# Optimization experiments

Hardware: AMD Instinct MI355X
Metric: run time of the kernel (lower is better)

## Reference

```python
import jax, jax.numpy as jnp
import numpy as np

B, N, F_IN, H = 16, 1024, 64, 256
NEG = -9e15
ALPHA = 0.2  # LeakyReLU slope


def _leaky(x):
    return jnp.where(x >= 0, x, ALPHA * x)


def setup_inputs() -> dict:
    key = jax.random.key(0)
    ks = jax.random.split(key, 12)
    s = lambda k, shape, fan: jax.random.normal(k, shape, jnp.float32) / np.sqrt(fan)
    node_features = jax.random.normal(ks[0], (B, N, F_IN), jnp.float32)
    adj_matrix = jax.random.randint(ks[1], (B, N, N), 0, 2).astype(jnp.float32)
    return {
        "node_features": node_features,
        "adj_matrix": adj_matrix,
        "emb_W": s(ks[2], (F_IN, H), F_IN),
        "emb_b": jnp.zeros((H,), jnp.float32),
        "W0": s(ks[3], (H, H), H),
        "a1_0": s(ks[4], (H,), H),
        "a2_0": s(ks[5], (H,), H),
        "W1": s(ks[6], (H, H), H),
        "a1_1": s(ks[7], (H,), H),
        "a2_1": s(ks[8], (H,), H),
        "gp_W1": s(ks[9], (H, H), H),
        "gp_b1": jnp.zeros((H,), jnp.float32),
        "gp_W2": s(ks[10], (H, H), H),
        "gp_b2": jnp.zeros((H,), jnp.float32),
    }


def _gat_layer(x, mask, W, a1, a2):
    # x: [B,N,H]; mask: [B,N,N] bool. Equivalent to original concat trick:
    # a([h_i || h_j]) = h_i @ a1 + h_j @ a2 with a.weight split in halves.
    h = jnp.einsum('bnf,fo->bno', x, W)              # [B,N,H]
    s1 = jnp.einsum('bnh,h->bn', h, a1)              # [B,N]
    s2 = jnp.einsum('bnh,h->bn', h, a2)              # [B,N]
    e = _leaky(s1[:, :, None] + s2[:, None, :])      # [B,N,N]
    att = jax.nn.softmax(jnp.where(mask, e, NEG), axis=2)
    # dropout p=0.2 is identity in eval mode
    return jnp.einsum('bij,bjh->bih', att, h)        # [B,N,H]


def reference(node_features, adj_matrix, emb_W, emb_b,
              W0, a1_0, a2_0, W1, a1_1, a2_1,
              gp_W1, gp_b1, gp_W2, gp_b2):
    mask = adj_matrix > 0
    x = jnp.einsum('bnf,fh->bnh', node_features, emb_W) + emb_b
    x = jax.nn.relu(_gat_layer(x, mask, W0, a1_0, a2_0))
    x = jax.nn.relu(_gat_layer(x, mask, W1, a1_1, a2_1))
    g = jnp.mean(x, axis=1) + jnp.max(x, axis=1)     # [B,H]
    g = jax.nn.relu(g @ gp_W1 + gp_b1) @ gp_W2 + gp_b2
    return x, g
```

## Files before the change

### kernel.cpp

```cpp
#include <hip/hip_runtime.h>
#include <hip/hip_bf16.h>

#define B 16
#define N 1024
#define F_IN 64
#define H 256
#define ALPHA 0.2f
#define LOG2E 1.44269504f

typedef __attribute__((ext_vector_type(8))) _Float16 half8;
typedef __attribute__((ext_vector_type(4))) _Float16 half4;
typedef __attribute__((ext_vector_type(4))) float floatx4;
typedef __attribute__((ext_vector_type(16))) float floatx16;

#if __has_builtin(__builtin_amdgcn_exp2f)
#define EXP2F(x) __builtin_amdgcn_exp2f(x)
#else
#define EXP2F(x) exp2f(x)
#endif

__device__ __forceinline__ floatx4 mfma_f16(half8 a, half8 b, floatx4 c) {
    return __builtin_amdgcn_mfma_f32_16x16x32_f16(a, b, c, 0, 0, 0);
}
__device__ __forceinline__ floatx16 mfma32_f16(half8 a, half8 b, floatx16 c) {
    return __builtin_amdgcn_mfma_f32_32x32x16_f16(a, b, c, 0, 0, 0);
}

__global__ __launch_bounds__(256) void k_prep(const float* __restrict__ embW,
                                              const float* __restrict__ W0, const float* __restrict__ W1,
                                              const float* __restrict__ a10, const float* __restrict__ a20,
                                              const float* __restrict__ a11, const float* __restrict__ a21,
                                              _Float16* __restrict__ wBf,
                                              _Float16* __restrict__ embf,
                                              float* __restrict__ wa1, float* __restrict__ wa2,
                                              int* __restrict__ cnt) {
    __shared__ float lds[256 * 17];
    const int blk = blockIdx.x;
    const int t = threadIdx.x;
    const int lane = t & 63;

    if (blk == 34) {
        if (t < B) cnt[t] = 0;
        for (int s = t; s < 2048; s += 256) {
            const int ln = s & 63, ct2 = s >> 6;
            const int ct = ct2 >> 1, ks2 = ct2 & 1;
            const int q = ln >> 4, lw = ln & 15;
            half8 bf;
#pragma unroll
            for (int e = 0; e < 8; e++)
                bf[e] = (_Float16)embW[(ks2 * 32 + q * 8 + e) * H + ct * 16 + lw];
            *(half8*)(embf + (size_t)s * 8) = bf;
        }
        return;
    }
    if (blk >= 32) {
        const int l = blk - 32;
        const float* W = l ? W1 : W0;
        const float* a1 = l ? a11 : a10;
        const float* a2 = l ? a21 : a20;
        float* a1s = lds;
        float* a2s = lds + 256;
        a1s[t] = a1[t]; a2s[t] = a2[t];
        __syncthreads();
        float v1 = 0.f, v2 = 0.f;
        for (int c = 0; c < H; c += 4) {
            float4 w = *(const float4*)&W[t * H + c];
            v1 += w.x * a1s[c] + w.y * a1s[c + 1] + w.z * a1s[c + 2] + w.w * a1s[c + 3];
            v2 += w.x * a2s[c] + w.y * a2s[c + 1] + w.z * a2s[c + 2] + w.w * a2s[c + 3];
        }
        wa1[l * H + t] = v1;
        wa2[l * H + t] = v2;
        return;
    }
    const int l = blk >> 4, ct = blk & 15;
    const float* W = l ? W1 : W0;
#pragma unroll
    for (int rep = 0; rep < 16; rep++) {
        int idx = rep * 256 + t;
        int k = idx >> 4, cl = idx & 15;
        lds[k * 17 + cl] = W[k * H + ct * 16 + cl];
    }
    __syncthreads();
    const int w = t >> 6;
    const int l15 = lane & 15, quad = lane >> 4;
#pragma unroll
    for (int e = 0; e < 2; e++) {
        const int ks = w * 2 + e;
        half8 bf;
#pragma unroll
        for (int jj = 0; jj < 8; jj++)
            bf[jj] = (_Float16)lds[(ks * 32 + quad * 8 + jj) * 17 + l15];
        *(half8*)(wBf + (size_t)(((l * 16 + ct) * 8 + ks) * 64 + lane) * 8) = bf;
    }
}

#define XS(it, ks) ((((it) * 8 + (ks))) * 520)
__global__ __launch_bounds__(256, 4) void k_mix(const float* __restrict__ adj,
                                                const float* __restrict__ nf,
                                                const _Float16* __restrict__ embf,
                                                const float* __restrict__ embB,
                                                const _Float16* __restrict__ wBf,
                                                const float* __restrict__ wa1, const float* __restrict__ wa2,
                                                unsigned* __restrict__ mask32,
                                                _Float16* __restrict__ hB,
                                                float* __restrict__ s1, float* __restrict__ s2) {
    __shared__ __align__(16) _Float16 sm[8320];
    const int blk = blockIdx.x;
    const int t = threadIdx.x;
    const int lane = t & 63;

    if (blk & 1) {
        const int id = blk >> 1;
        const int wv = id * 4 + (t >> 6);
#pragma unroll 2
        for (int task = wv; task < B * N * 4; task += 4096) {
            const float4 v = *(const float4*)(adj + (size_t)task * 256 + lane * 4);
            unsigned long long b0 = __ballot(v.x > 0.f);
            unsigned long long b1 = __ballot(v.y > 0.f);
            unsigned long long b2 = __ballot(v.z > 0.f);
            unsigned long long b3 = __ballot(v.w > 0.f);
            if (lane < 8) {
                unsigned w0 = (unsigned)((b0 >> (8 * lane)) & 0xff)
                            | ((unsigned)((b1 >> (8 * lane)) & 0xff) << 8)
                            | ((unsigned)((b2 >> (8 * lane)) & 0xff) << 16)
                            | ((unsigned)((b3 >> (8 * lane)) & 0xff) << 24);
                const int jg = task & 3, row = task >> 2;
                mask32[(size_t)row * 32 + jg * 8 + lane] = w0;
            }
        }
        return;
    }

    const int lin = blk >> 1;
    const int rc = lin >> 1, chalf = lin & 1;
    const int row0 = rc * 32;
    const int w = t >> 6;
    const int l15 = lane & 15, quad = lane >> 4;

    {
        half8 anf[2][2];
#pragma unroll
        for (int it = 0; it < 2; it++)
#pragma unroll
            for (int ks2 = 0; ks2 < 2; ks2++) {
                const float* src = nf + (size_t)(row0 + it * 16 + l15) * F_IN + ks2 * 32 + quad * 8;
                float4 f0 = *(const float4*)(src);
                float4 f1 = *(const float4*)(src + 4);
                half8 a;
                a[0] = (_Float16)f0.x; a[1] = (_Float16)f0.y;
                a[2] = (_Float16)f0.z; a[3] = (_Float16)f0.w;
                a[4] = (_Float16)f1.x; a[5] = (_Float16)f1.y;
                a[6] = (_Float16)f1.z; a[7] = (_Float16)f1.w;
                anf[it][ks2] = a;
            }
#pragma unroll
        for (int ctl = 0; ctl < 4; ctl++) {
            const int ct = w * 4 + ctl;
            half8 be0 = *(const half8*)(embf + (size_t)((ct * 2 + 0) * 64 + lane) * 8);
            half8 be1 = *(const half8*)(embf + (size_t)((ct * 2 + 1) * 64 + lane) * 8);
            const int col = ct * 16 + l15;
            const float bias = embB[col];
            const int ks = col >> 5, qd = (col >> 3) & 3, e = col & 7;
#pragma unroll
            for (int it = 0; it < 2; it++) {
                floatx4 xa = {0.f, 0.f, 0.f, 0.f};
                xa = mfma_f16(anf[it][0], be0, xa);
                xa = mfma_f16(anf[it][1], be1, xa);
#pragma unroll
                for (int r = 0; r < 4; r++)
                    sm[XS(it, ks) + (qd * 16 + quad * 4 + r) * 8 + e] = (_Float16)(xa[r] + bias);
            }
        }
    }
    __syncthreads();

    const int ct0 = chalf * 8 + 2 * w;
    const _Float16* pB0 = wBf + (size_t)((ct0 * 8) * 64 + lane) * 8;
    const _Float16* pB1 = wBf + (size_t)(((ct0 + 1) * 8) * 64 + lane) * 8;

    floatx4 acc[2][2];
    floatx4 z = {0.f, 0.f, 0.f, 0.f};
    acc[0][0] = z; acc[0][1] = z; acc[1][0] = z; acc[1][1] = z;
    float sp1a = 0.f, sp2a = 0.f, sp1b = 0.f, sp2b = 0.f;

    half8 B0 = *(const half8*)(pB0);
    half8 B1 = *(const half8*)(pB1);

#pragma unroll
    for (int ks = 0; ks < 8; ks++) {
        half8 nB0 = B0, nB1 = B1;
        if (ks < 7) {
            const int o = (ks + 1) * 512;
            nB0 = *(const half8*)(pB0 + o);
            nB1 = *(const half8*)(pB1 + o);
        }
        half8 A0 = *(const half8*)(sm + XS(0, ks) + lane * 8);
        half8 A1 = *(const half8*)(sm + XS(1, ks) + lane * 8);
        acc[0][0] = mfma_f16(A0, B0, acc[0][0]);
        acc[0][1] = mfma_f16(A0, B1, acc[0][1]);
        acc[1][0] = mfma_f16(A1, B0, acc[1][0]);
        acc[1][1] = mfma_f16(A1, B1, acc[1][1]);
        if (chalf == 0 && w == 0) {
            float4 w1a = *(const float4*)(wa1 + ks * 32 + quad * 8);
            float4 w1b = *(const float4*)(wa1 + ks * 32 + quad * 8 + 4);
            float4 w2a = *(const float4*)(wa2 + ks * 32 + quad * 8);
            float4 w2b = *(const float4*)(wa2 + ks * 32 + quad * 8 + 4);
            float wv1[8] = {w1a.x, w1a.y, w1a.z, w1a.w, w1b.x, w1b.y, w1b.z, w1b.w};
            float wv2[8] = {w2a.x, w2a.y, w2a.z, w2a.w, w2b.x, w2b.y, w2b.z, w2b.w};
#pragma unroll
            for (int j = 0; j < 8; j++) {
                float xa = (float)A0[j];
                float xb = (float)A1[j];
                sp1a += xa * wv1[j]; sp2a += xa * wv2[j];
                sp1b += xb * wv1[j]; sp2b += xb * wv2[j];
            }
        }
        B0 = nB0; B1 = nB1;
    }

    __syncthreads();
    _Float16* trc = sm;
#pragma unroll
    for (int rg = 0; rg < 2; rg++) {
#pragma unroll
        for (int n2 = 0; n2 < 2; n2++) {
            const int c_l = (2 * w + n2) * 16 + l15;
            half4 hv;
            hv[0] = (_Float16)acc[rg][n2][0];
            hv[1] = (_Float16)acc[rg][n2][1];
            hv[2] = (_Float16)acc[rg][n2][2];
            hv[3] = (_Float16)acc[rg][n2][3];
            *(half4*)(trc + c_l * 40 + rg * 16 + quad * 4) = hv;
        }
    }
    __syncthreads();
    {
        const int bb = row0 >> 10, jtb = (row0 >> 5) & 31;
#pragma unroll
        for (int rep = 0; rep < 2; rep++) {
            int slot = rep * 256 + t;
            int l = slot & 63, frag = slot >> 6;
            int k4 = frag >> 1, ks = frag & 1;
            int c_l = k4 * 32 + (l & 31);
            int roff = ks * 16 + (l >> 5) * 8;
            half8 hv = *(const half8*)(trc + c_l * 40 + roff);
            _Float16* dst = hB + ((size_t)((bb * 8 + chalf * 4 + k4) * 32 + jtb) * 2 + ks) * 512 + l * 8;
            *(half8*)dst = hv;
        }
    }
    if (chalf == 0 && w == 0) {
        sp1a += __shfl_xor(sp1a, 16); sp1a += __shfl_xor(sp1a, 32);
        sp2a += __shfl_xor(sp2a, 16); sp2a += __shfl_xor(sp2a, 32);
        sp1b += __shfl_xor(sp1b, 16); sp1b += __shfl_xor(sp1b, 32);
        sp2b += __shfl_xor(sp2b, 16); sp2b += __shfl_xor(sp2b, 32);
        if (quad == 0) {
            s1[row0 + l15] = sp1a; s2[row0 + l15] = sp2a;
            s1[row0 + 16 + l15] = sp1b; s2[row0 + 16 + l15] = sp2b;
        }
    }
}

__global__ __launch_bounds__(256, 4) void k_gemm(const _Float16* __restrict__ xf,
                                                 const _Float16* __restrict__ wBf,
                                                 const float* __restrict__ wa1, const float* __restrict__ wa2,
                                                 _Float16* __restrict__ hB,
                                                 float* __restrict__ s1, float* __restrict__ s2) {
    __shared__ __align__(16) _Float16 sm[8320];
    const int lin = blockIdx.x;
    const int rc = lin >> 1, chalf = lin & 1;
    const int row0 = rc * 32;
    const int t = threadIdx.x;
    const int lane = t & 63, w = t >> 6;
    const int l15 = lane & 15, quad = lane >> 4;

#pragma unroll
    for (int pass = 0; pass < 4; pass++) {
        int idx = pass * 256 + t;
        int row_l = idx >> 5, k8 = idx & 31;
        half8 v = *(const half8*)(xf + (size_t)(row0 + row_l) * H + k8 * 8);
        int it = row_l >> 4, lf = row_l & 15, ks = k8 >> 2, qd = k8 & 3;
        *(half8*)(sm + XS(it, ks) + (qd * 16 + lf) * 8) = v;
    }
    __syncthreads();

    const int ct0 = chalf * 8 + 2 * w;
    const _Float16* pB0 = wBf + (size_t)((ct0 * 8) * 64 + lane) * 8;
    const _Float16* pB1 = wBf + (size_t)(((ct0 + 1) * 8) * 64 + lane) * 8;

    floatx4 acc[2][2];
    floatx4 z = {0.f, 0.f, 0.f, 0.f};
    acc[0][0] = z; acc[0][1] = z; acc[1][0] = z; acc[1][1] = z;
    float sp1a = 0.f, sp2a = 0.f, sp1b = 0.f, sp2b = 0.f;

    half8 B0 = *(const half8*)(pB0);
    half8 B1 = *(const half8*)(pB1);

#pragma unroll
    for (int ks = 0; ks < 8; ks++) {
        half8 nB0 = B0, nB1 = B1;
        if (ks < 7) {
            const int o = (ks + 1) * 512;
            nB0 = *(const half8*)(pB0 + o);
            nB1 = *(const half8*)(pB1 + o);
        }
        half8 A0 = *(const half8*)(sm + XS(0, ks) + lane * 8);
        half8 A1 = *(const half8*)(sm + XS(1, ks) + lane * 8);
        acc[0][0] = mfma_f16(A0, B0, acc[0][0]);
        acc[0][1] = mfma_f16(A0, B1, acc[0][1]);
        acc[1][0] = mfma_f16(A1, B0, acc[1][0]);
        acc[1][1] = mfma_f16(A1, B1, acc[1][1]);
        if (chalf == 0 && w == 0) {
            float4 w1a = *(const float4*)(wa1 + ks * 32 + quad * 8);
            float4 w1b = *(const float4*)(wa1 + ks * 32 + quad * 8 + 4);
            float4 w2a = *(const float4*)(wa2 + ks * 32 + quad * 8);
            float4 w2b = *(const float4*)(wa2 + ks * 32 + quad * 8 + 4);
            float wv1[8] = {w1a.x, w1a.y, w1a.z, w1a.w, w1b.x, w1b.y, w1b.z, w1b.w};
            float wv2[8] = {w2a.x, w2a.y, w2a.z, w2a.w, w2b.x, w2b.y, w2b.z, w2b.w};
#pragma unroll
            for (int j = 0; j < 8; j++) {
                float xa = (float)A0[j];
                float xb = (float)A1[j];
                sp1a += xa * wv1[j]; sp2a += xa * wv2[j];
                sp1b += xb * wv1[j]; sp2b += xb * wv2[j];
            }
        }
        B0 = nB0; B1 = nB1;
    }

    __syncthreads();
    _Float16* trc = sm;
#pragma unroll
    for (int rg = 0; rg < 2; rg++) {
#pragma unroll
        for (int n2 = 0; n2 < 2; n2++) {
            const int c_l = (2 * w + n2) * 16 + l15;
            half4 hv;
            hv[0] = (_Float16)acc[rg][n2][0];
            hv[1] = (_Float16)acc[rg][n2][1];
            hv[2] = (_Float16)acc[rg][n2][2];
            hv[3] = (_Float16)acc[rg][n2][3];
            *(half4*)(trc + c_l * 40 + rg * 16 + quad * 4) = hv;
        }
    }
    __syncthreads();
    {
        const int bb = row0 >> 10, jtb = (row0 >> 5) & 31;
#pragma unroll
        for (int rep = 0; rep < 2; rep++) {
            int slot = rep * 256 + t;
            int l = slot & 63, frag = slot >> 6;
            int k4 = frag >> 1, ks = frag & 1;
            int c_l = k4 * 32 + (l & 31);
            int roff = ks * 16 + (l >> 5) * 8;
            half8 hv = *(const half8*)(trc + c_l * 40 + roff);
            _Float16* dst = hB + ((size_t)((bb * 8 + chalf * 4 + k4) * 32 + jtb) * 2 + ks) * 512 + l * 8;
            *(half8*)dst = hv;
        }
    }
    if (chalf == 0 && w == 0) {
        sp1a += __shfl_xor(sp1a, 16); sp1a += __shfl_xor(sp1a, 32);
        sp2a += __shfl_xor(sp2a, 16); sp2a += __shfl_xor(sp2a, 32);
        sp1b += __shfl_xor(sp1b, 16); sp1b += __shfl_xor(sp1b, 32);
        sp2b += __shfl_xor(sp2b, 16); sp2b += __shfl_xor(sp2b, 32);
        if (quad == 0) {
            s1[row0 + l15] = sp1a; s2[row0 + l15] = sp2a;
            s1[row0 + 16 + l15] = sp1b; s2[row0 + 16 + l15] = sp2b;
        }
    }
}

template <int LAST>
__global__ __launch_bounds__(256, 2) void k_gat(const _Float16* __restrict__ hB,
                                                const float* __restrict__ s1g,
                                                const float* __restrict__ s2g,
                                                const unsigned* __restrict__ mask32,
                                                float* __restrict__ outf,
                                                _Float16* __restrict__ oxf,
                                                float* __restrict__ psum, float* __restrict__ pmax,
                                                const float* __restrict__ gpW1, const float* __restrict__ gpb1,
                                                const float* __restrict__ gpW2, const float* __restrict__ gpb2,
                                                float* __restrict__ gout, int* __restrict__ cnt) {
    __shared__ float s2s[N];
    __shared__ unsigned msk[128][33];
    __shared__ float wmax[4];
    __shared__ float red1[4][64];
    __shared__ float red2[4][64];
    __shared__ int lastf;
    const int lin = blockIdx.x;
    const int xcd = lin & 7, sl = lin >> 3;
    const int b = xcd * 2 + (sl & 1);
    const int chunk = (sl >> 1) & 7;
    const int colq = sl >> 4;
    const int ctb = colq * 2;
    const int i0 = chunk * 128;
    const int t = threadIdx.x;
    const int lane = t & 63, w = t >> 6;
    const int l31 = lane & 31, hi = lane >> 5;
    const int hi2 = hi * 2, hi8 = hi * 8;

    float tm = -INFINITY;
    for (int idx = t; idx < N; idx += 256) {
        float v = s2g[b * N + idx] * LOG2E;
        s2s[idx] = v;
        tm = fmaxf(tm, v);
    }
#pragma unroll
    for (int off = 1; off <= 32; off <<= 1) tm = fmaxf(tm, __shfl_xor(tm, off));
    if (lane == 0) wmax[w] = tm;
#pragma unroll
    for (int pass = 0; pass < 16; pass++) {
        int idx = pass * 256 + t;
        int r = idx >> 5, wd = idx & 31;
        msk[r][wd] = mask32[(size_t)(b * N + i0 + r) * 32 + wd];
    }
    __syncthreads();
    const float s2maxL = fmaxf(fmaxf(wmax[0], wmax[1]), fmaxf(wmax[2], wmax[3]));

    const float s1L = s1g[b * N + i0 + w * 32 + l31] * LOG2E;
    const float tmx = s1L + s2maxL;
    const float mL = fmaxf(tmx, ALPHA * tmx);
    const float a1c = s1L - mL;
    const float a2c = fmaf(ALPHA, s1L, -mL);

    const _Float16* pb[2][2];
#pragma unroll
    for (int k2 = 0; k2 < 2; k2++)
#pragma unroll
        for (int ks = 0; ks < 2; ks++)
            pb[k2][ks] = hB + ((size_t)(b * 8 + ctb + k2) * 64 + ks) * 512 + lane * 8;

    floatx16 acc[2];
    floatx16 accl;
#pragma unroll
    for (int r = 0; r < 16; r++) accl[r] = 0.f;
    acc[0] = accl; acc[1] = accl;

    half8 ones;
#pragma unroll
    for (int jj = 0; jj < 8; jj++) ones[jj] = (_Float16)1.0f;

    const float* svp = s2s + hi8;
    const unsigned* mr = &msk[w * 32 + l31][0];

    half8 bufA[2][2], bufB[2][2];
#pragma unroll
    for (int k2 = 0; k2 < 2; k2++) {
        bufA[k2][0] = *(const half8*)(pb[k2][0]);
        bufA[k2][1] = *(const half8*)(pb[k2][1]);
    }

#define GAT_STEP(JT, BUF)                                                      \
    do {                                                                       \
        const unsigned m = mr[JT];                                             \
        float4 sa0 = *(const float4*)(svp + (JT) * 32);                        \
        float4 sb0 = *(const float4*)(svp + (JT) * 32 + 4);                    \
        float4 sa1 = *(const float4*)(svp + (JT) * 32 + 16);                   \
        float4 sb1 = *(const float4*)(svp + (JT) * 32 + 20);                   \
        float sv0[8] = {sa0.x, sa0.y, sa0.z, sa0.w, sb0.x, sb0.y, sb0.z, sb0.w};\
        float sv1[8] = {sa1.x, sa1.y, sa1.z, sa1.w, sb1.x, sb1.y, sb1.z, sb1.w};\
        unsigned mq0 = m >> hi2;                                               \
        unsigned mq1 = m >> (4 + hi2);                                         \
        union { _Float16 h[8]; half8 v; } pk0, pk1;                            \
        _Pragma("unroll")                                                      \
        for (int e = 0; e < 8; e++) {                                          \
            const int bp = (e & 3) * 8 + (e >> 2);                             \
            float u0 = a1c + sv0[e];                                           \
            float v0 = fmaf(ALPHA, sv0[e], a2c);                               \
            float w0 = fmaxf(u0, v0);                                          \
            w0 = ((mq0 >> bp) & 1u) ? w0 : -126.f;                             \
            pk0.h[e] = (_Float16)EXP2F(w0);                                    \
            float u1 = a1c + sv1[e];                                           \
            float v1 = fmaf(ALPHA, sv1[e], a2c);                               \
            float w1 = fmaxf(u1, v1);                                          \
            w1 = ((mq1 >> bp) & 1u) ? w1 : -126.f;                             \
            pk1.h[e] = (_Float16)EXP2F(w1);                                    \
        }                                                                      \
        accl = mfma32_f16(pk0.v, ones, accl);                                  \
        acc[0] = mfma32_f16(pk0.v, BUF[0][0], acc[0]);                         \
        acc[1] = mfma32_f16(pk0.v, BUF[1][0], acc[1]);                         \
        accl = mfma32_f16(pk1.v, ones, accl);                                  \
        acc[0] = mfma32_f16(pk1.v, BUF[0][1], acc[0]);                         \
        acc[1] = mfma32_f16(pk1.v, BUF[1][1], acc[1]);                         \
    } while (0)

    for (int jt = 0; jt < 32; jt += 2) {
        {
            const int o = (jt + 1) * 1024;
#pragma unroll
            for (int k2 = 0; k2 < 2; k2++) {
                bufB[k2][0] = *(const half8*)(pb[k2][0] + o);
                bufB[k2][1] = *(const half8*)(pb[k2][1] + o);
            }
        }
        GAT_STEP(jt, bufA);
        if (jt + 2 < 32) {
            const int o = (jt + 2) * 1024;
#pragma unroll
            for (int k2 = 0; k2 < 2; k2++) {
                bufA[k2][0] = *(const half8*)(pb[k2][0] + o);
                bufA[k2][1] = *(const half8*)(pb[k2][1] + o);
            }
        }
        GAT_STEP(jt + 1, bufB);
    }
#undef GAT_STEP

    float invv[16];
#pragma unroll
    for (int r = 0; r < 16; r++) invv[r] = 1.f / accl[r];

    const size_t rowb = (size_t)b * N + i0 + w * 32 + 4 * hi;
#pragma unroll
    for (int k2 = 0; k2 < 2; k2++) {
        const int c = colq * 64 + k2 * 32 + l31;
        float cs = 0.f, cm = -INFINITY;
#pragma unroll
        for (int reg = 0; reg < 16; reg++) {
            const int roff = (reg & 3) + 8 * (reg >> 2);
            float v = fmaxf(acc[k2][reg] * invv[reg], 0.f);
            if (LAST) {
                outf[(rowb + roff) * H + c] = v;
                cs += v; cm = fmaxf(cm, v);
            } else {
                oxf[(rowb + roff) * H + c] = (_Float16)v;
            }
        }
        if (LAST) {
            cs += __shfl_xor(cs, 32);
            cm = fmaxf(cm, __shfl_xor(cm, 32));
            if (hi == 0) { red1[w][k2 * 32 + l31] = cs; red2[w][k2 * 32 + l31] = cm; }
        }
    }
    if (LAST) {
        __syncthreads();
        if (t < 64) {
            float s = red1[0][t] + red1[1][t] + red1[2][t] + red1[3][t];
            float m = fmaxf(fmaxf(red2[0][t], red2[1][t]), fmaxf(red2[2][t], red2[3][t]));
            __hip_atomic_store(&psum[(b * 8 + chunk) * H + colq * 64 + t], s,
                               __ATOMIC_RELAXED, __HIP_MEMORY_SCOPE_AGENT);
            __hip_atomic_store(&pmax[(b * 8 + chunk) * H + colq * 64 + t], m,
                               __ATOMIC_RELAXED, __HIP_MEMORY_SCOPE_AGENT);
        }
        asm volatile("s_waitcnt vmcnt(0)" ::: "memory");
        __syncthreads();
        if (t == 0) {
            int old = atomicAdd(&cnt[b], 1);
            lastf = (old == 31) ? 1 : 0;
        }
        __syncthreads();
        if (lastf) {
            float* g_s = s2s;
            float* t_s = s2s + 256;
            const int c = t;
            float s = 0.f, m = -INFINITY;
#pragma unroll
            for (int ch = 0; ch < 8; ch++) {
                s += __hip_atomic_load(&psum[(b * 8 + ch) * H + c],
                                       __ATOMIC_RELAXED, __HIP_MEMORY_SCOPE_AGENT);
                m = fmaxf(m, __hip_atomic_load(&pmax[(b * 8 + ch) * H + c],
                                               __ATOMIC_RELAXED, __HIP_MEMORY_SCOPE_AGENT));
            }
            g_s[c] = s * (1.f / N) + m;
            __syncthreads();
            float a = gpb1[c];
#pragma unroll 16
            for (int k = 0; k < H; k++) a += g_s[k] * gpW1[k * H + c];
            t_s[c] = fmaxf(a, 0.f);
            __syncthreads();
            float o = gpb2[c];
#pragma unroll 16
            for (int k = 0; k < H; k++) o += t_s[k] * gpW2[k * H + c];
            gout[b * H + c] = o;
        }
    }
}

extern "C" void kernel_launch(void* const* d_in, const int* in_sizes, int n_in,
                              void* d_out, int out_size, void* d_ws, size_t ws_size,
                              hipStream_t stream) {
    const float* nf    = (const float*)d_in[0];
    const float* adj   = (const float*)d_in[1];
    const float* emb_W = (const float*)d_in[2];
    const float* emb_b = (const float*)d_in[3];
    const float* W0    = (const float*)d_in[4];
    const float* a1_0  = (const float*)d_in[5];
    const float* a2_0  = (const float*)d_in[6];
    const float* W1    = (const float*)d_in[7];
    const float* a1_1  = (const float*)d_in[8];
    const float* a2_1  = (const float*)d_in[9];
    const float* gpW1  = (const float*)d_in[10];
    const float* gpb1  = (const float*)d_in[11];
    const float* gpW2  = (const float*)d_in[12];
    const float* gpb2  = (const float*)d_in[13];

    float* xout = (float*)d_out;
    float* gout = xout + B * N * H;

    char* w = (char*)d_ws;
    _Float16* xf     = (_Float16*)(w);
    _Float16* hB     = (_Float16*)(w + 8388608);
    unsigned* mask32 = (unsigned*)(w + 16777216);
    float* s1        = (float*)(w + 18874368);
    float* s2        = (float*)(w + 18939904);
    _Float16* wBf    = (_Float16*)(w + 19005440);
    float* wa1       = (float*)(w + 19267584);
    float* wa2       = (float*)(w + 19269632);
    float* psum      = (float*)(w + 19271680);
    float* pmax      = (float*)(w + 19533824);
    _Float16* embf   = (_Float16*)(w + 19795968);
    int* cnt         = (int*)(w + 19828736);

    k_prep<<<35, 256, 0, stream>>>(emb_W, W0, W1, a1_0, a2_0, a1_1, a2_1,
                                   wBf, embf, wa1, wa2, cnt);

    k_mix<<<2048, 256, 0, stream>>>(adj, nf, embf, emb_b, wBf, wa1, wa2,
                                    mask32, hB, s1, s2);
    k_gat<0><<<512, 256, 0, stream>>>(hB, s1, s2, mask32, nullptr, xf,
                                      nullptr, nullptr, nullptr, nullptr,
                                      nullptr, nullptr, nullptr, nullptr);

    k_gemm<<<1024, 256, 0, stream>>>(xf, wBf + 65536, wa1 + H, wa2 + H, hB, s1, s2);
    k_gat<1><<<512, 256, 0, stream>>>(hB, s1, s2, mask32, xout, nullptr,
                                      psum, pmax, gpW1, gpb1, gpW2, gpb2,
                                      gout, cnt);
}
```

Measured before the change: 225.8 us.

## Split GAT key dimension across two wave groups and combine partials in LDS

After: 223.4 us. Within noise of the previous version (-1.1%).

```diff
diff --git a/kernel.cpp b/kernel.cpp
--- a/kernel.cpp
+++ b/kernel.cpp
@@ -370,7 +370,7 @@
 }
 
 template <int LAST>
-__global__ __launch_bounds__(256, 2) void k_gat(const _Float16* __restrict__ hB,
+__global__ __launch_bounds__(512, 4) void k_gat(const _Float16* __restrict__ hB,
                                                 const float* __restrict__ s1g,
                                                 const float* __restrict__ s2g,
                                                 const unsigned* __restrict__ mask32,
@@ -382,7 +382,8 @@
                                                 float* __restrict__ gout, int* __restrict__ cnt) {
     __shared__ float s2s[N];
     __shared__ unsigned msk[128][33];
-    __shared__ float wmax[4];
+    __shared__ float wmax[8];
+    __shared__ float comb[4][32][64];
     __shared__ float red1[4][64];
     __shared__ float red2[4][64];
     __shared__ int lastf;
@@ -394,29 +395,32 @@
     const int ctb = colq * 2;
     const int i0 = chunk * 128;
     const int t = threadIdx.x;
-    const int lane = t & 63, w = t >> 6;
+    const int lane = t & 63, w8 = t >> 6;
+    const int wi = w8 & 3, jh = w8 >> 2;
     const int l31 = lane & 31, hi = lane >> 5;
     const int hi2 = hi * 2, hi8 = hi * 8;
 
     float tm = -INFINITY;
-    for (int idx = t; idx < N; idx += 256) {
+    for (int idx = t; idx < N; idx += 512) {
         float v = s2g[b * N + idx] * LOG2E;
         s2s[idx] = v;
         tm = fmaxf(tm, v);
     }
 #pragma unroll
     for (int off = 1; off <= 32; off <<= 1) tm = fmaxf(tm, __shfl_xor(tm, off));
-    if (lane == 0) wmax[w] = tm;
-#pragma unroll
-    for (int pass = 0; pass < 16; pass++) {
-        int idx = pass * 256 + t;
+    if (lane == 0) wmax[w8] = tm;
+#pragma unroll
+    for (int pass = 0; pass < 8; pass++) {
+        int idx = pass * 512 + t;
         int r = idx >> 5, wd = idx & 31;
         msk[r][wd] = mask32[(size_t)(b * N + i0 + r) * 32 + wd];
     }
     __syncthreads();
-    const float s2maxL = fmaxf(fmaxf(wmax[0], wmax[1]), fmaxf(wmax[2], wmax[3]));
-
-    const float s1L = s1g[b * N + i0 + w * 32 + l31] * LOG2E;
+    float s2maxL = wmax[0];
+#pragma unroll
+    for (int q = 1; q < 8; q++) s2maxL = fmaxf(s2maxL, wmax[q]);
+
+    const float s1L = s1g[b * N + i0 + wi * 32 + l31] * LOG2E;
     const float tmx = s1L + s2maxL;
     const float mL = fmaxf(tmx, ALPHA * tmx);
     const float a1c = s1L - mL;
@@ -440,13 +444,14 @@
     for (int jj = 0; jj < 8; jj++) ones[jj] = (_Float16)1.0f;
 
     const float* svp = s2s + hi8;
-    const unsigned* mr = &msk[w * 32 + l31][0];
-
+    const unsigned* mr = &msk[wi * 32 + l31][0];
+
+    const int jt0 = jh * 16;
     half8 bufA[2][2], bufB[2][2];
 #pragma unroll
     for (int k2 = 0; k2 < 2; k2++) {
-        bufA[k2][0] = *(const half8*)(pb[k2][0]);
-        bufA[k2][1] = *(const half8*)(pb[k2][1]);
+        bufA[k2][0] = *(const half8*)(pb[k2][0] + jt0 * 1024);
+        bufA[k2][1] = *(const half8*)(pb[k2][1] + jt0 * 1024);
     }
 
 #define GAT_STEP(JT, BUF)                                                      \
@@ -483,7 +488,8 @@
         acc[1] = mfma32_f16(pk1.v, BUF[1][1], acc[1]);                         \
     } while (0)
 
-    for (int jt = 0; jt < 32; jt += 2) {
+    for (int jt2 = 0; jt2 < 16; jt2 += 2) {
+        const int jt = jt0 + jt2;
         {
             const int o = (jt + 1) * 1024;
 #pragma unroll
@@ -493,7 +499,7 @@
             }
         }
         GAT_STEP(jt, bufA);
-        if (jt + 2 < 32) {
+        if (jt2 + 2 < 16) {
             const int o = (jt + 2) * 1024;
 #pragma unroll
             for (int k2 = 0; k2 < 2; k2++) {
@@ -505,30 +511,54 @@
     }
 #undef GAT_STEP
 
-    float invv[16];
-#pragma unroll
-    for (int r = 0; r < 16; r++) invv[r] = 1.f / accl[r];
-
-    const size_t rowb = (size_t)b * N + i0 + w * 32 + 4 * hi;
-#pragma unroll
-    for (int k2 = 0; k2 < 2; k2++) {
-        const int c = colq * 64 + k2 * 32 + l31;
-        float cs = 0.f, cm = -INFINITY;
-#pragma unroll
-        for (int reg = 0; reg < 16; reg++) {
-            const int roff = (reg & 3) + 8 * (reg >> 2);
-            float v = fmaxf(acc[k2][reg] * invv[reg], 0.f);
+    if (jh == 1) {
+#pragma unroll
+        for (int r = 0; r < 16; r++) {
+            comb[wi][r][lane] = acc[0][r];
+            comb[wi][16 + r][lane] = acc[1][r];
+        }
+    }
+    __syncthreads();
+    if (jh == 0) {
+#pragma unroll
+        for (int r = 0; r < 16; r++) {
+            acc[0][r] += comb[wi][r][lane];
+            acc[1][r] += comb[wi][16 + r][lane];
+        }
+    }
+    __syncthreads();
+    if (jh == 1) {
+#pragma unroll
+        for (int r = 0; r < 16; r++) comb[wi][r][lane] = accl[r];
+    }
+    __syncthreads();
+
+    if (jh == 0) {
+        float invv[16];
+#pragma unroll
+        for (int r = 0; r < 16; r++) invv[r] = 1.f / (accl[r] + comb[wi][r][lane]);
+
+        const size_t rowb = (size_t)b * N + i0 + wi * 32 + 4 * hi;
+#pragma unroll
+        for (int k2 = 0; k2 < 2; k2++) {
+            const int c = colq * 64 + k2 * 32 + l31;
+            float cs = 0.f, cm = -INFINITY;
+#pragma unroll
+            for (int reg = 0; reg < 16; reg++) {
+                const int roff = (reg & 3) + 8 * (reg >> 2);
+                float v = fmaxf(acc[k2][reg] * invv[reg], 0.f);
+                if (LAST) {
+                    outf[(rowb + roff) * H + c] = v;
+                    cs += v; cm = fmaxf(cm, v);
+                } else {
+                    oxf[(rowb + roff) * H + c] = (_Float16)v;
+                }
+            }
             if (LAST) {
-                outf[(rowb + roff) * H + c] = v;
-                cs += v; cm = fmaxf(cm, v);
-            } else {
-                oxf[(rowb + roff) * H + c] = (_Float16)v;
-            }
-        }
-        if (LAST) {
-            cs += __shfl_xor(cs, 32);
-            cm = fmaxf(cm, __shfl_xor(cm, 32));
-            if (hi == 0) { red1[w][k2 * 32 + l31] = cs; red2[w][k2 * 32 + l31] = cm; }
+                cs += __shfl_xor(cs, 32);
+                cm = fmaxf(cm, __shfl_xor(cm, 32));
+                if (hi == 0) { red1[wi][k2 * 32 + l31] = cs; red2[wi][k2 * 32 + l31] = cm; }
+            }
         }
     }
     if (LAST) {
@@ -552,25 +582,31 @@
             float* g_s = s2s;
             float* t_s = s2s + 256;
             const int c = t;
-            float s = 0.f, m = -INFINITY;
-#pragma unroll
-            for (int ch = 0; ch < 8; ch++) {
-                s += __hip_atomic_load(&psum[(b * 8 + ch) * H + c],
-                                       __ATOMIC_RELAXED, __HIP_MEMORY_SCOPE_AGENT);
-                m = fmaxf(m, __hip_atomic_load(&pmax[(b * 8 + ch) * H + c],
-                                               __ATOMIC_RELAXED, __HIP_MEMORY_SCOPE_AGENT));
-            }
-            g_s[c] = s * (1.f / N) + m;
+            if (c < H) {
+                float s = 0.f, m = -INFINITY;
+#pragma unroll
+                for (int ch = 0; ch < 8; ch++) {
+                    s += __hip_atomic_load(&psum[(b * 8 + ch) * H + c],
+                                           __ATOMIC_RELAXED, __HIP_MEMORY_SCOPE_AGENT);
+                    m = fmaxf(m, __hip_atomic_load(&pmax[(b * 8 + ch) * H + c],
+                                                   __ATOMIC_RELAXED, __HIP_MEMORY_SCOPE_AGENT));
+                }
+                g_s[c] = s * (1.f / N) + m;
+            }
             __syncthreads();
-            float a = gpb1[c];
+            if (c < H) {
+                float a = gpb1[c];
 #pragma unroll 16
-            for (int k = 0; k < H; k++) a += g_s[k] * gpW1[k * H + c];
-            t_s[c] = fmaxf(a, 0.f);
+                for (int k = 0; k < H; k++) a += g_s[k] * gpW1[k * H + c];
+                t_s[c] = fmaxf(a, 0.f);
+            }
             __syncthreads();
-            float o = gpb2[c];
+            if (c < H) {
+                float o = gpb2[c];
 #pragma unroll 16
-            for (int k = 0; k < H; k++) o += t_s[k] * gpW2[k * H + c];
-            gout[b * H + c] = o;
+                for (int k = 0; k < H; k++) o += t_s[k] * gpW2[k * H + c];
+                gout[b * H + c] = o;
+            }
         }
     }
 }
@@ -615,12 +651,12 @@
 
     k_mix<<<2048, 256, 0, stream>>>(adj, nf, embf, emb_b, wBf, wa1, wa2,
                                     mask32, hB, s1, s2);
-    k_gat<0><<<512, 256, 0, stream>>>(hB, s1, s2, mask32, nullptr, xf,
+    k_gat<0><<<512, 512, 0, stream>>>(hB, s1, s2, mask32, nullptr, xf,
                                       nullptr, nullptr, nullptr, nullptr,
                                       nullptr, nullptr, nullptr, nullptr);
 
     k_gemm<<<1024, 256, 0, stream>>>(xf, wBf + 65536, wa1 + H, wa2 + H, hB, s1, s2);
-    k_gat<1><<<512, 256, 0, stream>>>(hB, s1, s2, mask32, xout, nullptr,
+    k_gat<1><<<512, 512, 0, stream>>>(hB, s1, s2, mask32, xout, nullptr,
                                       psum, pmax, gpW1, gpb1, gpW2, gpb2,
                                       gout, cnt);
 }
```
